# Optimization experiments

Hardware: AMD Instinct MI355X
Metric: run time of the kernel (lower is better)

The kernel has to match this reference:

```python
import jax, jax.numpy as jnp
import numpy as np
import math

N_HEADS = 16

def _rope_tables(T, D, dtype):
    # inv_freq over even dims, emb = [freqs, freqs] -> [T, D]
    inv_freq = 1.0 / (10000.0 ** (jnp.arange(0, D, 2, dtype=jnp.float32) / D))
    freqs = jnp.arange(T, dtype=jnp.float32)[:, None] * inv_freq[None, :]  # [T, D/2]
    emb = jnp.concatenate([freqs, freqs], axis=-1)  # [T, D]
    return jnp.cos(emb).astype(dtype), jnp.sin(emb).astype(dtype)

def _rotate_half(x):
    d = x.shape[-1] // 2
    return jnp.concatenate([-x[..., d:], x[..., :d]], axis=-1)

def setup_inputs() -> dict:
    key = jax.random.key(0)
    ks = jax.random.split(key, 5)
    B, T, C = 2, 2048, 1024
    s = 1.0 / math.sqrt(C)
    return {
        "x": jax.random.normal(ks[0], (B, T, C), dtype=jnp.float32),
        "Wq": jax.random.normal(ks[1], (C, C), dtype=jnp.float32) * s,
        "Wk": jax.random.normal(ks[2], (C, C), dtype=jnp.float32) * s,
        "Wv": jax.random.normal(ks[3], (C, C), dtype=jnp.float32) * s,
        "Wo": jax.random.normal(ks[4], (C, C), dtype=jnp.float32) * s,
    }

def reference(x, Wq, Wk, Wv, Wo):
    B, T, C = x.shape
    H = N_HEADS
    D = C // H
    # QKV projections (torch Linear, bias=False: y = x @ W.T), split into heads
    def proj(W):
        return (x @ W.T).reshape(B, T, H, D).transpose(0, 2, 1, 3)  # [B,H,T,D]
    q, k, v = proj(Wq), proj(Wk), proj(Wv)
    # RoPE
    cos, sin = _rope_tables(T, D, x.dtype)  # [T,D] each, broadcast over B,H
    q = q * cos + _rotate_half(q) * sin
    k = k * cos + _rotate_half(k) * sin
    # scaled dot-product attention with causal mask
    scale = 1.0 / math.sqrt(D)
    attn = jnp.einsum('bhtd,bhsd->bhts', q, k) * scale  # [B,H,T,T]
    row = jnp.arange(T)[:, None]
    col = jnp.arange(T)[None, :]
    attn = jnp.where(col > row, -jnp.inf, attn)
    p = jax.nn.softmax(attn, axis=-1)
    out = jnp.einsum('bhts,bhsd->bhtd', p, v)  # [B,H,T,D]
    out = out.transpose(0, 2, 1, 3).reshape(B, T, C)
    return out @ Wo.T
```

## Files before the change

kernel.cpp:

```cpp
#include <hip/hip_runtime.h>
#include <hip/hip_bf16.h>


typedef __hip_bfloat16 bf16;
typedef __attribute__((ext_vector_type(8))) short bf16x8;
typedef __attribute__((ext_vector_type(4))) float f32x4;
typedef __attribute__((ext_vector_type(4))) short short4v;

#define MFMA16(a, b, c) __builtin_amdgcn_mfma_f32_16x16x32_bf16((a), (b), (c), 0, 0, 0)

constexpr int Bn = 2, Hn = 16, Tn = 2048, Dn = 64, Cn = 1024;
constexpr size_t NE = (size_t)Bn * Tn * Cn;
constexpr size_t WE = (size_t)Cn * Cn;

__device__ inline unsigned short bfbits(float x) {
    bf16 b = __float2bfloat16(x);
    return *(unsigned short*)&b;
}

__device__ inline bf16x8 pack8(f32x4 a, f32x4 b) {
    bf16x8 r;
#pragma unroll
    for (int i = 0; i < 4; ++i) r[i] = (short)bfbits(a[i]);
#pragma unroll
    for (int i = 0; i < 4; ++i) r[4 + i] = (short)bfbits(b[i]);
    return r;
}

__device__ inline void gl_lds16(const bf16* g, unsigned short* l) {
    __builtin_amdgcn_global_load_lds(
        (const __attribute__((address_space(1))) void*)g,
        (__attribute__((address_space(3))) void*)l, 16, 0, 0);
}

__device__ inline void stage128(const bf16* gbase, int ld, unsigned short* lds,
                                int wave, int lane) {
#pragma unroll
    for (int j = 0; j < 4; ++j) {
        int p = j * 256 + wave * 64 + lane;
        int row = p >> 3, ch = (p & 7) ^ (row & 7);
        gl_lds16(gbase + (size_t)row * ld + ch * 8,
                 lds + (size_t)(j * 256 + wave * 64) * 8);
    }
}
__device__ inline void stage64(const bf16* gbase, int ld, unsigned short* lds,
                               int wave, int lane) {
#pragma unroll
    for (int j = 0; j < 2; ++j) {
        int p = j * 256 + wave * 64 + lane;
        int row = p >> 3, ch = (p & 7) ^ (row & 7);
        gl_lds16(gbase + (size_t)row * ld + ch * 8,
                 lds + (size_t)(j * 256 + wave * 64) * 8);
    }
}

__device__ inline bf16x8 ldsfrag(const unsigned short* base, int row, int ch) {
    return *(const bf16x8*)&base[row * 64 + ((ch ^ (row & 7)) * 8)];
}

__global__ __launch_bounds__(256) void convert_kernel(
    const float* __restrict__ x, const float* __restrict__ wq,
    const float* __restrict__ wk, const float* __restrict__ wv,
    const float* __restrict__ wo, bf16* __restrict__ dst)
{
    int blk = blockIdx.x;
    if (blk < 2048) {
        const float* src = x + (size_t)blk * 2048;
        int t = threadIdx.x * 8;
        f32x4 a = *(const f32x4*)(src + t);
        f32x4 b2 = *(const f32x4*)(src + t + 4);
        *(bf16x8*)(dst + (size_t)blk * 2048 + t) = pack8(a, b2);
    } else {
        int w = (blk - 2048) >> 9, b = (blk - 2048) & 511;
        const float* s4[4] = {wq, wk, wv, wo};
        const float* W = s4[w];
        int frag = b * 4 + (threadIdx.x >> 6);
        int lane = threadIdx.x & 63;
        int lx = lane & 15, quad = lane >> 4;
        int nb = frag >> 5, kc = frag & 31;
        const float* src = W + (size_t)(nb * 16 + lx) * Cn + kc * 32 + quad * 8;
        f32x4 a = *(const f32x4*)(src);
        f32x4 b2 = *(const f32x4*)(src + 4);
        *(bf16x8*)(dst + NE + (size_t)w * WE + (size_t)frag * 512 + lane * 8) =
            pack8(a, b2);
    }
}

__global__ __launch_bounds__(256) void gemm_qkv_kernel(
    const bf16* __restrict__ X, const bf16* __restrict__ Wbase,
    bf16* __restrict__ Qo, bf16* __restrict__ Ko, bf16* __restrict__ Vo)
{
    __shared__ unsigned short As[128 * 64];
    const int bm = blockIdx.x, bn = blockIdx.y, wsel = blockIdx.z;
    const bf16* W = Wbase + (size_t)wsel * WE;
    const int tid  = threadIdx.x;
    const int wave = tid >> 6, lane = tid & 63;
    const int lx   = lane & 15, quad = lane >> 4;
    const int wm = wave >> 1, wn = wave & 1;

    const bf16* abase = X + (size_t)(bm * 128) * Cn;
    const int nb0 = bn * 8 + wn * 4;
    const bf16* wfrag = W + (size_t)nb0 * 32 * 512 + (size_t)lane * 8;

    f32x4 acc[4][4] = {};
    for (int kt = 0; kt < Cn / 64; ++kt) {
        __syncthreads();
        stage128(abase + kt * 64, Cn, As, wave, lane);
        bf16x8 bfv[4][2];
#pragma unroll
        for (int nt = 0; nt < 4; ++nt)
#pragma unroll
            for (int ks = 0; ks < 2; ++ks)
                bfv[nt][ks] = *(const bf16x8*)(wfrag +
                    ((size_t)nt * 32 + kt * 2 + ks) * 512);
        __syncthreads();
#pragma unroll
        for (int ks = 0; ks < 2; ++ks) {
            bf16x8 af[4];
#pragma unroll
            for (int mt = 0; mt < 4; ++mt)
                af[mt] = ldsfrag(As, wm * 64 + mt * 16 + lx, ks * 4 + quad);
#pragma unroll
            for (int mt = 0; mt < 4; ++mt)
#pragma unroll
                for (int nt = 0; nt < 4; ++nt)
                    acc[mt][nt] = MFMA16(af[mt], bfv[nt][ks], acc[mt][nt]);
        }
    }

    const int h = bn * 2 + wn;
    if (wsel <= 1) {
#pragma unroll
        for (int mt = 0; mt < 4; ++mt)
#pragma unroll
            for (int r = 0; r < 4; ++r) {
                int mg = bm * 128 + wm * 64 + mt * 16 + quad * 4 + r;
                int t  = mg & (Tn - 1);
#pragma unroll
                for (int nt = 0; nt < 2; ++nt) {
                    int d = nt * 16 + lx;
                    float ang = (float)t * __expf(-(float)d * 0.2878231366f);
                    float c, s;
                    __sincosf(ang, &s, &c);
                    float a0 = acc[mt][nt][r], a1 = acc[mt][nt + 2][r];
                    acc[mt][nt][r]     = a0 * c - a1 * s;
                    acc[mt][nt + 2][r] = a1 * c + a0 * s;
                }
            }
    }

#pragma unroll
    for (int mt = 0; mt < 4; ++mt) {
        int mg0 = bm * 128 + wm * 64 + mt * 16 + quad * 4;
        int b = mg0 >> 11, t0 = mg0 & (Tn - 1);
        if (wsel == 0) {
#pragma unroll
            for (int nt = 0; nt < 4; ++nt)
#pragma unroll
                for (int r = 0; r < 4; ++r) {
                    int d = nt * 16 + lx;
                    Qo[((size_t)(b * Hn + h) * Tn + t0 + r) * Dn + d] =
                        __float2bfloat16(acc[mt][nt][r] * 0.125f);
                }
        } else if (wsel == 1) {
#pragma unroll
            for (int nt = 0; nt < 4; ++nt)
#pragma unroll
                for (int r = 0; r < 4; ++r) {
                    int d = nt * 16 + lx;
                    Ko[((size_t)(b * Hn + h) * Tn + t0 + r) * Dn + d] =
                        __float2bfloat16(acc[mt][nt][r]);
                }
        } else {
#pragma unroll
            for (int nt = 0; nt < 4; ++nt) {
                int d = nt * 16 + lx;
                short4v pk;
#pragma unroll
                for (int r = 0; r < 4; ++r) pk[r] = (short)bfbits(acc[mt][nt][r]);
                *(short4v*)&Vo[((size_t)(b * Hn + h) * Dn + d) * Tn + t0] = pk;
            }
        }
    }
}

__global__ __launch_bounds__(256) void gemm_out_kernel(
    const bf16* __restrict__ A, const bf16* __restrict__ W, float* __restrict__ Out)
{
    __shared__ unsigned short As[128 * 64];
    const int bm = blockIdx.x, bn = blockIdx.y;
    const int tid  = threadIdx.x;
    const int wave = tid >> 6, lane = tid & 63;
    const int lx   = lane & 15, quad = lane >> 4;
    const int wm = wave >> 1, wn = wave & 1;

    const bf16* abase = A + (size_t)(bm * 128) * Cn;
    const int nb0 = bn * 4 + wn * 2;
    const bf16* wfrag = W + (size_t)nb0 * 32 * 512 + (size_t)lane * 8;

    f32x4 acc[4][2] = {};
    for (int kt = 0; kt < Cn / 64; ++kt) {
        __syncthreads();
        stage128(abase + kt * 64, Cn, As, wave, lane);
        bf16x8 bfv[2][2];
#pragma unroll
        for (int nt = 0; nt < 2; ++nt)
#pragma unroll
            for (int ks = 0; ks < 2; ++ks)
                bfv[nt][ks] = *(const bf16x8*)(wfrag +
                    ((size_t)nt * 32 + kt * 2 + ks) * 512);
        __syncthreads();
#pragma unroll
        for (int ks = 0; ks < 2; ++ks) {
            bf16x8 af[4];
#pragma unroll
            for (int mt = 0; mt < 4; ++mt)
                af[mt] = ldsfrag(As, wm * 64 + mt * 16 + lx, ks * 4 + quad);
#pragma unroll
            for (int mt = 0; mt < 4; ++mt)
#pragma unroll
                for (int nt = 0; nt < 2; ++nt)
                    acc[mt][nt] = MFMA16(af[mt], bfv[nt][ks], acc[mt][nt]);
        }
    }
#pragma unroll
    for (int mt = 0; mt < 4; ++mt)
#pragma unroll
        for (int nt = 0; nt < 2; ++nt)
#pragma unroll
            for (int r = 0; r < 4; ++r) {
                int mg = bm * 128 + wm * 64 + mt * 16 + quad * 4 + r;
                int ng = bn * 64 + wn * 32 + nt * 16 + lx;
                Out[(size_t)mg * Cn + ng] = acc[mt][nt][r];
            }
}

__global__ __launch_bounds__(256) void attn_kernel(
    const bf16* __restrict__ Q, const bf16* __restrict__ K,
    const bf16* __restrict__ Vt, bf16* __restrict__ O)
{
    __shared__ unsigned short Ks[64 * 64];
    __shared__ unsigned short Vs[64 * 64];
    __shared__ unsigned short Pl[4][16 * 72];
    const int f  = blockIdx.x;
    const int bh = (f & 7) * 4 + ((f >> 3) & 3);
    const int qb = 31 - (f >> 5);
    const int tid  = threadIdx.x;
    const int wave = tid >> 6, lane = tid & 63;
    const int lx   = lane & 15, quad = lane >> 4;

    const bf16* Qh = Q  + (size_t)bh * Tn * Dn;
    const bf16* Kh = K  + (size_t)bh * Tn * Dn;
    const bf16* Vh = Vt + (size_t)bh * Dn * Tn;
    unsigned short* pw = &Pl[wave][0];

    const int qrowA = qb * 64 + wave * 16 + lx;
    bf16x8 aq0 = *(const bf16x8*)(Qh + (size_t)qrowA * Dn + quad * 8);
    bf16x8 aq1 = *(const bf16x8*)(Qh + (size_t)qrowA * Dn + 32 + quad * 8);

    bf16x8 ones;
#pragma unroll
    for (int i = 0; i < 8; ++i) ones[i] = (short)0x3F80;

    f32x4 acc_o[4] = {};
    f32x4 acc_l = {};
    const int row_local = wave * 16 + quad * 4;

    for (int c = 0; c <= qb; ++c) {
        __syncthreads();
        stage64(Kh + (size_t)c * 64 * Dn, Dn, Ks, wave, lane);
        stage64(Vh + (size_t)c * 64, Tn, Vs, wave, lane);
        __syncthreads();
        f32x4 accs[4] = {};
#pragma unroll
        for (int nt = 0; nt < 4; ++nt) {
            int key = nt * 16 + lx;
            bf16x8 k0 = ldsfrag(Ks, key, quad);
            bf16x8 k1 = ldsfrag(Ks, key, quad + 4);
            accs[nt] = MFMA16(aq0, k0, accs[nt]);
            accs[nt] = MFMA16(aq1, k1, accs[nt]);
        }
        if (c < qb) {
#pragma unroll
            for (int nt = 0; nt < 4; ++nt)
#pragma unroll
                for (int r = 0; r < 4; ++r)
                    pw[(quad * 4 + r) * 72 + nt * 16 + lx] = bfbits(__expf(accs[nt][r]));
        } else {
#pragma unroll
            for (int nt = 0; nt < 4; ++nt) {
                int keyl = nt * 16 + lx;
#pragma unroll
                for (int r = 0; r < 4; ++r) {
                    float p = (keyl > row_local + r) ? 0.0f : __expf(accs[nt][r]);
                    pw[(quad * 4 + r) * 72 + nt * 16 + lx] = bfbits(p);
                }
            }
        }
        asm volatile("s_waitcnt lgkmcnt(0)" ::: "memory");
        bf16x8 ap0 = *(const bf16x8*)&pw[lx * 72 + quad * 8];
        bf16x8 ap1 = *(const bf16x8*)&pw[lx * 72 + 32 + quad * 8];
        acc_l = MFMA16(ap0, ones, acc_l);
        acc_l = MFMA16(ap1, ones, acc_l);
#pragma unroll
        for (int dt = 0; dt < 4; ++dt) {
            int d = dt * 16 + lx;
            bf16x8 v0 = ldsfrag(Vs, d, quad);
            bf16x8 v1 = ldsfrag(Vs, d, quad + 4);
            acc_o[dt] = MFMA16(ap0, v0, acc_o[dt]);
            acc_o[dt] = MFMA16(ap1, v1, acc_o[dt]);
        }
    }

    const int b = bh >> 4, h = bh & 15;
#pragma unroll
    for (int dt = 0; dt < 4; ++dt)
#pragma unroll
        for (int r = 0; r < 4; ++r) {
            int t = qb * 64 + row_local + r;
            int d = dt * 16 + lx;
            float o = acc_o[dt][r] / acc_l[r];
            O[((size_t)(b * Tn + t) * Hn + h) * Dn + d] = __float2bfloat16(o);
        }
}

extern "C" void kernel_launch(void* const* d_in, const int* in_sizes, int n_in,
                              void* d_out, int out_size, void* d_ws, size_t ws_size,
                              hipStream_t stream)
{
    const float* x  = (const float*)d_in[0];
    const float* Wq = (const float*)d_in[1];
    const float* Wk = (const float*)d_in[2];
    const float* Wv = (const float*)d_in[3];
    const float* Wo = (const float*)d_in[4];
    float* out = (float*)d_out;

    bf16* ws = (bf16*)d_ws;
    bf16* Xb = ws;
    bf16* Wb = ws + NE;
    bf16* Qb = ws + NE + 4 * WE;
    bf16* Kb = Qb + NE;
    bf16* Vb = Kb + NE;
    bf16* Ab = Xb;

    convert_kernel<<<4096, 256, 0, stream>>>(x, Wq, Wk, Wv, Wo, ws);
    gemm_qkv_kernel<<<dim3(32, 8, 3), 256, 0, stream>>>(Xb, Wb, Qb, Kb, Vb);
    attn_kernel<<<1024, 256, 0, stream>>>(Qb, Kb, Vb, Ab);
    gemm_out_kernel<<<dim3(32, 16), 256, 0, stream>>>(Ab, Wb + 3 * WE, out);
}
```

Measured before the change: 178.5 us.

## Pair causal query tiles per block and share staged K/V chunks

```diff
diff --git a/kernel.cpp b/kernel.cpp
--- a/kernel.cpp
+++ b/kernel.cpp
@@ -12,6 +12,7 @@
 constexpr int Bn = 2, Hn = 16, Tn = 2048, Dn = 64, Cn = 1024;
 constexpr size_t NE = (size_t)Bn * Tn * Cn;
 constexpr size_t WE = (size_t)Cn * Cn;
+constexpr float QSCALE = 0.125f * 1.44269504088896f;
 
 __device__ inline unsigned short bfbits(float x) {
     bf16 b = __float2bfloat16(x);
@@ -160,7 +161,7 @@
                 for (int r = 0; r < 4; ++r) {
                     int d = nt * 16 + lx;
                     Qo[((size_t)(b * Hn + h) * Tn + t0 + r) * Dn + d] =
-                        __float2bfloat16(acc[mt][nt][r] * 0.125f);
+                        __float2bfloat16(acc[mt][nt][r] * QSCALE);
                 }
         } else if (wsel == 1) {
 #pragma unroll
@@ -235,16 +236,99 @@
             }
 }
 
+__device__ inline void attn_chunk(
+    const unsigned short* Ks, const unsigned short* Vs,
+    unsigned short* phi, unsigned short* plo,
+    bf16x8 aqhi0, bf16x8 aqhi1, bf16x8 aqlo0, bf16x8 aqlo1, bf16x8 ones,
+    f32x4 (&acc_o)[2][4], f32x4 (&acc_l)[2],
+    int row_local, bool mask_hi, bool do_lo, bool mask_lo, int lx, int quad)
+{
+    f32x4 shi[4] = {}, slo[4] = {};
+#pragma unroll
+    for (int nt = 0; nt < 4; ++nt) {
+        int key = nt * 16 + lx;
+        bf16x8 k0 = ldsfrag(Ks, key, quad);
+        bf16x8 k1 = ldsfrag(Ks, key, quad + 4);
+        shi[nt] = MFMA16(aqhi0, k0, shi[nt]);
+        shi[nt] = MFMA16(aqhi1, k1, shi[nt]);
+        if (do_lo) {
+            slo[nt] = MFMA16(aqlo0, k0, slo[nt]);
+            slo[nt] = MFMA16(aqlo1, k1, slo[nt]);
+        }
+    }
+    if (!mask_hi) {
+#pragma unroll
+        for (int nt = 0; nt < 4; ++nt)
+#pragma unroll
+            for (int r = 0; r < 4; ++r)
+                phi[(quad * 4 + r) * 72 + nt * 16 + lx] = bfbits(exp2f(shi[nt][r]));
+    } else {
+#pragma unroll
+        for (int nt = 0; nt < 4; ++nt) {
+            int keyl = nt * 16 + lx;
+#pragma unroll
+            for (int r = 0; r < 4; ++r) {
+                float p = (keyl > row_local + r) ? 0.0f : exp2f(shi[nt][r]);
+                phi[(quad * 4 + r) * 72 + nt * 16 + lx] = bfbits(p);
+            }
+        }
+    }
+    if (do_lo) {
+        if (!mask_lo) {
+#pragma unroll
+            for (int nt = 0; nt < 4; ++nt)
+#pragma unroll
+                for (int r = 0; r < 4; ++r)
+                    plo[(quad * 4 + r) * 72 + nt * 16 + lx] = bfbits(exp2f(slo[nt][r]));
+        } else {
+#pragma unroll
+            for (int nt = 0; nt < 4; ++nt) {
+                int keyl = nt * 16 + lx;
+#pragma unroll
+                for (int r = 0; r < 4; ++r) {
+                    float p = (keyl > row_local + r) ? 0.0f : exp2f(slo[nt][r]);
+                    plo[(quad * 4 + r) * 72 + nt * 16 + lx] = bfbits(p);
+                }
+            }
+        }
+    }
+    asm volatile("s_waitcnt lgkmcnt(0)" ::: "memory");
+    bf16x8 aph0 = *(const bf16x8*)&phi[lx * 72 + quad * 8];
+    bf16x8 aph1 = *(const bf16x8*)&phi[lx * 72 + 32 + quad * 8];
+    acc_l[0] = MFMA16(aph0, ones, acc_l[0]);
+    acc_l[0] = MFMA16(aph1, ones, acc_l[0]);
+    bf16x8 apl0, apl1;
+    if (do_lo) {
+        apl0 = *(const bf16x8*)&plo[lx * 72 + quad * 8];
+        apl1 = *(const bf16x8*)&plo[lx * 72 + 32 + quad * 8];
+        acc_l[1] = MFMA16(apl0, ones, acc_l[1]);
+        acc_l[1] = MFMA16(apl1, ones, acc_l[1]);
+    }
+#pragma unroll
+    for (int dt = 0; dt < 4; ++dt) {
+        int d = dt * 16 + lx;
+        bf16x8 v0 = ldsfrag(Vs, d, quad);
+        bf16x8 v1 = ldsfrag(Vs, d, quad + 4);
+        acc_o[0][dt] = MFMA16(aph0, v0, acc_o[0][dt]);
+        acc_o[0][dt] = MFMA16(aph1, v1, acc_o[0][dt]);
+        if (do_lo) {
+            acc_o[1][dt] = MFMA16(apl0, v0, acc_o[1][dt]);
+            acc_o[1][dt] = MFMA16(apl1, v1, acc_o[1][dt]);
+        }
+    }
+}
+
 __global__ __launch_bounds__(256) void attn_kernel(
     const bf16* __restrict__ Q, const bf16* __restrict__ K,
     const bf16* __restrict__ Vt, bf16* __restrict__ O)
 {
-    __shared__ unsigned short Ks[64 * 64];
-    __shared__ unsigned short Vs[64 * 64];
-    __shared__ unsigned short Pl[4][16 * 72];
-    const int f  = blockIdx.x;
-    const int bh = (f & 7) * 4 + ((f >> 3) & 3);
-    const int qb = 31 - (f >> 5);
+    __shared__ unsigned short Ks[2][64 * 64];
+    __shared__ unsigned short Vs[2][64 * 64];
+    __shared__ unsigned short Pl[2][4][16 * 72];
+    const int f = blockIdx.x;
+    const int bh   = (f & 7) * 4 + (f >> 7);
+    const int pair = (f >> 3) & 15;
+    const int qlo = pair, qhi = 31 - pair;
     const int tid  = threadIdx.x;
     const int wave = tid >> 6, lane = tid & 63;
     const int lx   = lane & 15, quad = lane >> 4;
@@ -252,76 +336,57 @@
     const bf16* Qh = Q  + (size_t)bh * Tn * Dn;
     const bf16* Kh = K  + (size_t)bh * Tn * Dn;
     const bf16* Vh = Vt + (size_t)bh * Dn * Tn;
-    unsigned short* pw = &Pl[wave][0];
-
-    const int qrowA = qb * 64 + wave * 16 + lx;
-    bf16x8 aq0 = *(const bf16x8*)(Qh + (size_t)qrowA * Dn + quad * 8);
-    bf16x8 aq1 = *(const bf16x8*)(Qh + (size_t)qrowA * Dn + 32 + quad * 8);
+    unsigned short* phi = &Pl[0][wave][0];
+    unsigned short* plo = &Pl[1][wave][0];
+
+    const int rlo = qlo * 64 + wave * 16 + lx;
+    const int rhi = qhi * 64 + wave * 16 + lx;
+    bf16x8 aqlo0 = *(const bf16x8*)(Qh + (size_t)rlo * Dn + quad * 8);
+    bf16x8 aqlo1 = *(const bf16x8*)(Qh + (size_t)rlo * Dn + 32 + quad * 8);
+    bf16x8 aqhi0 = *(const bf16x8*)(Qh + (size_t)rhi * Dn + quad * 8);
+    bf16x8 aqhi1 = *(const bf16x8*)(Qh + (size_t)rhi * Dn + 32 + quad * 8);
 
     bf16x8 ones;
 #pragma unroll
     for (int i = 0; i < 8; ++i) ones[i] = (short)0x3F80;
 
-    f32x4 acc_o[4] = {};
-    f32x4 acc_l = {};
+    f32x4 acc_o[2][4] = {};
+    f32x4 acc_l[2] = {};
     const int row_local = wave * 16 + quad * 4;
 
-    for (int c = 0; c <= qb; ++c) {
-        __syncthreads();
-        stage64(Kh + (size_t)c * 64 * Dn, Dn, Ks, wave, lane);
-        stage64(Vh + (size_t)c * 64, Tn, Vs, wave, lane);
-        __syncthreads();
-        f32x4 accs[4] = {};
-#pragma unroll
-        for (int nt = 0; nt < 4; ++nt) {
-            int key = nt * 16 + lx;
-            bf16x8 k0 = ldsfrag(Ks, key, quad);
-            bf16x8 k1 = ldsfrag(Ks, key, quad + 4);
-            accs[nt] = MFMA16(aq0, k0, accs[nt]);
-            accs[nt] = MFMA16(aq1, k1, accs[nt]);
-        }
-        if (c < qb) {
-#pragma unroll
-            for (int nt = 0; nt < 4; ++nt)
-#pragma unroll
-                for (int r = 0; r < 4; ++r)
-                    pw[(quad * 4 + r) * 72 + nt * 16 + lx] = bfbits(__expf(accs[nt][r]));
-        } else {
-#pragma unroll
-            for (int nt = 0; nt < 4; ++nt) {
-                int keyl = nt * 16 + lx;
-#pragma unroll
-                for (int r = 0; r < 4; ++r) {
-                    float p = (keyl > row_local + r) ? 0.0f : __expf(accs[nt][r]);
-                    pw[(quad * 4 + r) * 72 + nt * 16 + lx] = bfbits(p);
-                }
-            }
-        }
-        asm volatile("s_waitcnt lgkmcnt(0)" ::: "memory");
-        bf16x8 ap0 = *(const bf16x8*)&pw[lx * 72 + quad * 8];
-        bf16x8 ap1 = *(const bf16x8*)&pw[lx * 72 + 32 + quad * 8];
-        acc_l = MFMA16(ap0, ones, acc_l);
-        acc_l = MFMA16(ap1, ones, acc_l);
-#pragma unroll
-        for (int dt = 0; dt < 4; ++dt) {
-            int d = dt * 16 + lx;
-            bf16x8 v0 = ldsfrag(Vs, d, quad);
-            bf16x8 v1 = ldsfrag(Vs, d, quad + 4);
-            acc_o[dt] = MFMA16(ap0, v0, acc_o[dt]);
-            acc_o[dt] = MFMA16(ap1, v1, acc_o[dt]);
-        }
+    for (int c = 0; c <= qhi; c += 2) {
+        const bool two = (c + 1 <= qhi);
+        __syncthreads();
+        stage64(Kh + (size_t)c * 64 * Dn, Dn, Ks[0], wave, lane);
+        stage64(Vh + (size_t)c * 64, Tn, Vs[0], wave, lane);
+        if (two) {
+            stage64(Kh + (size_t)(c + 1) * 64 * Dn, Dn, Ks[1], wave, lane);
+            stage64(Vh + (size_t)(c + 1) * 64, Tn, Vs[1], wave, lane);
+        }
+        __syncthreads();
+        attn_chunk(Ks[0], Vs[0], phi, plo, aqhi0, aqhi1, aqlo0, aqlo1, ones,
+                   acc_o, acc_l, row_local,
+                   c == qhi, c <= qlo, c == qlo, lx, quad);
+        if (two)
+            attn_chunk(Ks[1], Vs[1], phi, plo, aqhi0, aqhi1, aqlo0, aqlo1, ones,
+                       acc_o, acc_l, row_local,
+                       c + 1 == qhi, c + 1 <= qlo, c + 1 == qlo, lx, quad);
     }
 
     const int b = bh >> 4, h = bh & 15;
 #pragma unroll
-    for (int dt = 0; dt < 4; ++dt)
-#pragma unroll
-        for (int r = 0; r < 4; ++r) {
-            int t = qb * 64 + row_local + r;
-            int d = dt * 16 + lx;
-            float o = acc_o[dt][r] / acc_l[r];
-            O[((size_t)(b * Tn + t) * Hn + h) * Dn + d] = __float2bfloat16(o);
-        }
+    for (int tile = 0; tile < 2; ++tile) {
+        int qb = tile ? qlo : qhi;
+#pragma unroll
+        for (int dt = 0; dt < 4; ++dt)
+#pragma unroll
+            for (int r = 0; r < 4; ++r) {
+                int t = qb * 64 + wave * 16 + quad * 4 + r;
+                int d = dt * 16 + lx;
+                float o = acc_o[tile][dt][r] / acc_l[tile][r];
+                O[((size_t)(b * Tn + t) * Hn + h) * Dn + d] = __float2bfloat16(o);
+            }
+    }
 }
 
 extern "C" void kernel_launch(void* const* d_in, const int* in_sizes, int n_in,
@@ -345,6 +410,6 @@
 
     convert_kernel<<<4096, 256, 0, stream>>>(x, Wq, Wk, Wv, Wo, ws);
     gemm_qkv_kernel<<<dim3(32, 8, 3), 256, 0, stream>>>(Xb, Wb, Qb, Kb, Vb);
-    attn_kernel<<<1024, 256, 0, stream>>>(Qb, Kb, Vb, Ab);
+    attn_kernel<<<512, 256, 0, stream>>>(Qb, Kb, Vb, Ab);
     gemm_out_kernel<<<dim3(32, 16), 256, 0, stream>>>(Ab, Wb + 3 * WE, out);
 }
```

Result: slower. 190.3 us (+6.6%).

## Pre-fragment X for QKV GEMM, drop LDS staging, fold log2e into Q scale

Applied to the files above, without the earlier changes.

```diff
diff --git a/kernel.cpp b/kernel.cpp
--- a/kernel.cpp
+++ b/kernel.cpp
@@ -12,6 +12,7 @@
 constexpr int Bn = 2, Hn = 16, Tn = 2048, Dn = 64, Cn = 1024;
 constexpr size_t NE = (size_t)Bn * Tn * Cn;
 constexpr size_t WE = (size_t)Cn * Cn;
+constexpr float QSCALE = 0.125f * 1.44269504088896f;
 
 __device__ inline unsigned short bfbits(float x) {
     bf16 b = __float2bfloat16(x);
@@ -64,33 +65,32 @@
     const float* __restrict__ wo, bf16* __restrict__ dst)
 {
     int blk = blockIdx.x;
+    int lane = threadIdx.x & 63;
+    int lx = lane & 15, quad = lane >> 4;
+    const float* src;
+    size_t doff;
     if (blk < 2048) {
-        const float* src = x + (size_t)blk * 2048;
-        int t = threadIdx.x * 8;
-        f32x4 a = *(const f32x4*)(src + t);
-        f32x4 b2 = *(const f32x4*)(src + t + 4);
-        *(bf16x8*)(dst + (size_t)blk * 2048 + t) = pack8(a, b2);
+        int frag = blk * 4 + (threadIdx.x >> 6);
+        int mt = frag >> 5, kc = frag & 31;
+        src = x + (size_t)(mt * 16 + lx) * Cn + kc * 32 + quad * 8;
+        doff = (size_t)frag * 512 + lane * 8;
     } else {
         int w = (blk - 2048) >> 9, b = (blk - 2048) & 511;
         const float* s4[4] = {wq, wk, wv, wo};
-        const float* W = s4[w];
         int frag = b * 4 + (threadIdx.x >> 6);
-        int lane = threadIdx.x & 63;
-        int lx = lane & 15, quad = lane >> 4;
         int nb = frag >> 5, kc = frag & 31;
-        const float* src = W + (size_t)(nb * 16 + lx) * Cn + kc * 32 + quad * 8;
-        f32x4 a = *(const f32x4*)(src);
-        f32x4 b2 = *(const f32x4*)(src + 4);
-        *(bf16x8*)(dst + NE + (size_t)w * WE + (size_t)frag * 512 + lane * 8) =
-            pack8(a, b2);
-    }
+        src = s4[w] + (size_t)(nb * 16 + lx) * Cn + kc * 32 + quad * 8;
+        doff = NE + (size_t)w * WE + (size_t)frag * 512 + lane * 8;
+    }
+    f32x4 a = *(const f32x4*)(src);
+    f32x4 b2 = *(const f32x4*)(src + 4);
+    *(bf16x8*)(dst + doff) = pack8(a, b2);
 }
 
 __global__ __launch_bounds__(256) void gemm_qkv_kernel(
-    const bf16* __restrict__ X, const bf16* __restrict__ Wbase,
+    const bf16* __restrict__ Xf, const bf16* __restrict__ Wbase,
     bf16* __restrict__ Qo, bf16* __restrict__ Ko, bf16* __restrict__ Vo)
 {
-    __shared__ unsigned short As[128 * 64];
     const int bm = blockIdx.x, bn = blockIdx.y, wsel = blockIdx.z;
     const bf16* W = Wbase + (size_t)wsel * WE;
     const int tid  = threadIdx.x;
@@ -98,34 +98,33 @@
     const int lx   = lane & 15, quad = lane >> 4;
     const int wm = wave >> 1, wn = wave & 1;
 
-    const bf16* abase = X + (size_t)(bm * 128) * Cn;
+    const int mt0 = bm * 8 + wm * 4;
     const int nb0 = bn * 8 + wn * 4;
+    const bf16* afrag = Xf + (size_t)mt0 * 32 * 512 + (size_t)lane * 8;
     const bf16* wfrag = W + (size_t)nb0 * 32 * 512 + (size_t)lane * 8;
 
     f32x4 acc[4][4] = {};
-    for (int kt = 0; kt < Cn / 64; ++kt) {
-        __syncthreads();
-        stage128(abase + kt * 64, Cn, As, wave, lane);
-        bf16x8 bfv[4][2];
-#pragma unroll
-        for (int nt = 0; nt < 4; ++nt)
-#pragma unroll
-            for (int ks = 0; ks < 2; ++ks)
-                bfv[nt][ks] = *(const bf16x8*)(wfrag +
-                    ((size_t)nt * 32 + kt * 2 + ks) * 512);
-        __syncthreads();
-#pragma unroll
-        for (int ks = 0; ks < 2; ++ks) {
-            bf16x8 af[4];
-#pragma unroll
-            for (int mt = 0; mt < 4; ++mt)
-                af[mt] = ldsfrag(As, wm * 64 + mt * 16 + lx, ks * 4 + quad);
-#pragma unroll
-            for (int mt = 0; mt < 4; ++mt)
-#pragma unroll
-                for (int nt = 0; nt < 4; ++nt)
-                    acc[mt][nt] = MFMA16(af[mt], bfv[nt][ks], acc[mt][nt]);
-        }
+    bf16x8 acur[4], bcur[4], anxt[4], bnxt[4];
+#pragma unroll
+    for (int i = 0; i < 4; ++i) {
+        acur[i] = *(const bf16x8*)(afrag + (size_t)i * 32 * 512);
+        bcur[i] = *(const bf16x8*)(wfrag + (size_t)i * 32 * 512);
+    }
+    for (int kc = 0; kc < 32; ++kc) {
+        if (kc < 31) {
+#pragma unroll
+            for (int i = 0; i < 4; ++i) {
+                anxt[i] = *(const bf16x8*)(afrag + ((size_t)i * 32 + kc + 1) * 512);
+                bnxt[i] = *(const bf16x8*)(wfrag + ((size_t)i * 32 + kc + 1) * 512);
+            }
+        }
+#pragma unroll
+        for (int mt = 0; mt < 4; ++mt)
+#pragma unroll
+            for (int nt = 0; nt < 4; ++nt)
+                acc[mt][nt] = MFMA16(acur[mt], bcur[nt], acc[mt][nt]);
+#pragma unroll
+        for (int i = 0; i < 4; ++i) { acur[i] = anxt[i]; bcur[i] = bnxt[i]; }
     }
 
     const int h = bn * 2 + wn;
@@ -160,7 +159,7 @@
                 for (int r = 0; r < 4; ++r) {
                     int d = nt * 16 + lx;
                     Qo[((size_t)(b * Hn + h) * Tn + t0 + r) * Dn + d] =
-                        __float2bfloat16(acc[mt][nt][r] * 0.125f);
+                        __float2bfloat16(acc[mt][nt][r] * QSCALE);
                 }
         } else if (wsel == 1) {
 #pragma unroll
@@ -285,14 +284,14 @@
             for (int nt = 0; nt < 4; ++nt)
 #pragma unroll
                 for (int r = 0; r < 4; ++r)
-                    pw[(quad * 4 + r) * 72 + nt * 16 + lx] = bfbits(__expf(accs[nt][r]));
+                    pw[(quad * 4 + r) * 72 + nt * 16 + lx] = bfbits(exp2f(accs[nt][r]));
         } else {
 #pragma unroll
             for (int nt = 0; nt < 4; ++nt) {
                 int keyl = nt * 16 + lx;
 #pragma unroll
                 for (int r = 0; r < 4; ++r) {
-                    float p = (keyl > row_local + r) ? 0.0f : __expf(accs[nt][r]);
+                    float p = (keyl > row_local + r) ? 0.0f : exp2f(accs[nt][r]);
                     pw[(quad * 4 + r) * 72 + nt * 16 + lx] = bfbits(p);
                 }
             }
@@ -336,15 +335,15 @@
     float* out = (float*)d_out;
 
     bf16* ws = (bf16*)d_ws;
-    bf16* Xb = ws;
+    bf16* Xf = ws;
     bf16* Wb = ws + NE;
     bf16* Qb = ws + NE + 4 * WE;
     bf16* Kb = Qb + NE;
     bf16* Vb = Kb + NE;
-    bf16* Ab = Xb;
+    bf16* Ab = Xf;
 
     convert_kernel<<<4096, 256, 0, stream>>>(x, Wq, Wk, Wv, Wo, ws);
-    gemm_qkv_kernel<<<dim3(32, 8, 3), 256, 0, stream>>>(Xb, Wb, Qb, Kb, Vb);
+    gemm_qkv_kernel<<<dim3(32, 8, 3), 256, 0, stream>>>(Xf, Wb, Qb, Kb, Vb);
     attn_kernel<<<1024, 256, 0, stream>>>(Qb, Kb, Vb, Ab);
     gemm_out_kernel<<<dim3(32, 16), 256, 0, stream>>>(Ab, Wb + 3 * WE, out);
 }
```

New measurement: 177.2 us. Within noise of the previous version (-0.8%).
